# Kernel optimization log

Hardware: AMD Instinct MI355X
Metric: run time of the kernel (lower is better)

## Reference

```python
import jax, jax.numpy as jnp
import numpy as np

# Uniform batch of B graphs, N nodes each, C features, skip-window size FS
B, N, C, FS = 64, 512, 128, 16
RES = N - 1            # number of window rows per graph (unfold1d with stride 1)
TAU_A, TAU_B, TOT_EPOCHS = 10.0, 0.1, 100.0
EPS = 1e-20
NEG = -1e9


def setup_inputs() -> dict:
    key = jax.random.key(0)
    k1, k2, k3, k4 = jax.random.split(key, 4)
    x = jax.random.normal(k1, (B * N, C), dtype=jnp.float32)
    edge_index = jax.random.randint(k2, (2, 524288), 0, B * N, dtype=jnp.int32)
    score_w = jax.random.normal(k3, (C, 1), dtype=jnp.float32)       # TopKPool Linear weight
    att_params = jax.random.normal(k4, (2 * C, 1), dtype=jnp.float32)  # SKipPool att_params
    return {"x": x, "edge_index": edge_index, "score_w": score_w,
            "att_params": att_params, "epoch": 10}


def _forward(x, score_w, att_params, epoch):
    tau0 = TAU_A * (TAU_B / TAU_A) ** (epoch / TOT_EPOCHS)

    # ---- TopKPool scorer (init_ratio -> 1.0: keep all nodes, rank-sort per graph) ----
    scores = (x @ score_w)[:, 0] / jnp.linalg.norm(score_w)   # [B*N]
    sv = scores.reshape(B, N)
    order = jnp.argsort(-sv, axis=1)                           # descending perm per graph
    xg = jnp.take_along_axis(x.reshape(B, N, C), order[:, :, None], axis=1)  # [B,N,C]
    scores_ranked = jnp.tanh(jnp.take_along_axis(sv, order, axis=1))         # [B,N]

    # ---- skip-window edge construction (unfold1d semantics): row r -> dests r..r+FS-1 ----
    r = jnp.arange(RES)
    j = jnp.arange(FS)
    dest = r[:, None] + j[None, :]            # [RES,FS]
    valid = dest < N                          # padded positions masked (inf/zero rows)
    destc = jnp.minimum(dest, N - 1)

    xs = xg[:, :RES, None, :]                                  # [B,RES,1,C] sources
    xd = jnp.where(valid[None, :, :, None], xg[:, destc], 0.0)  # [B,RES,FS,C] dests

    # getDM_ei: RBF kernel over edge distances (sigma=1); masked edges -> 0 (inf row)
    d = jnp.linalg.norm(xs - xd, axis=-1)                      # [B,RES,FS]
    kmat = jnp.where(valid[None], jnp.exp(-d / 2.0), 0.0) - EPS

    # getSM_ei: attention score via att_params on [x_src || x_dst]
    a_src, a_dst = att_params[:C, 0], att_params[C:, 0]
    atts = (xg[:, :RES] @ a_src)[:, :, None] + jnp.einsum('brjc,c->brj', xd, a_dst)
    atts = jnp.where(valid[None], atts, NEG)
    w_att = jax.nn.softmax(atts / tau0, axis=-1)               # tau-annealed row softmax

    q = kmat * w_att                                           # combined edge score [B,RES,FS]
    qm = jnp.where(valid[None], q, NEG)
    w_row = jnp.max(qm, axis=-1)                               # best-match score per row (scatterSort top-1)
    jumps = 1 + jnp.argmax(qm[:, :, 1:], axis=-1).astype(jnp.int32)  # data-dependent stride in [1,FS-1]

    # ---- sequential pivot chaining (innerLoopStar): pivot -> pivot + jump[pivot] ----
    def chain(xg_b, w_b, sr_b, jumps_b):
        def step(carry, _):
            p, acc = carry
            active = p < RES
            pc = jnp.minimum(p, RES - 1)
            wv = jnp.where(active, w_b[pc] * sr_b[pc], 0.0)
            acc = acc + wv * xg_b[pc]
            p = jnp.where(active, p + jumps_b[pc], p)
            return (p, acc), None
        (pf, acc), _ = jax.lax.scan(step, (jnp.int32(0), jnp.zeros((C,), xg_b.dtype)),
                                    None, length=RES)
        return acc

    pooled = jax.vmap(chain)(xg, w_row, scores_ranked[:, :RES], jumps)  # [B,C]
    return pooled


def reference(x, edge_index, score_w, att_params, epoch):
    # edge_index only feeds the scorer's filter_adj in the original (structure unused here)
    return _forward(x, score_w, att_params, epoch)
```

## Files before the change

### kernel.cpp

```cpp
#include <hip/hip_runtime.h>
#include <math.h>

#define B_   64
#define N_   512
#define C_   128
#define FS_  16
#define RES_ 511
#define CHUNK_ 64
#define HALO_  15
#define MAXR_  (CHUNK_ + HALO_)
#define RSTRIDE_ 132

__device__ __forceinline__ float bf2f(unsigned short u) {
  union { unsigned int i; float f; } v;
  v.i = ((unsigned int)u) << 16;
  return v.f;
}

__device__ __forceinline__ float2 ld2(const void* p, int idx, int mode) {
  if (mode) return ((const float2*)p)[idx];
  ushort2 u = ((const ushort2*)p)[idx];
  return make_float2(bf2f(u.x), bf2f(u.y));
}
__device__ __forceinline__ float ld1(const void* p, int idx, int mode) {
  if (mode) return ((const float*)p)[idx];
  return bf2f(((const unsigned short*)p)[idx]);
}
__device__ __forceinline__ float4 ld4(const void* p, int idx4, int mode) {
  if (mode) return ((const float4*)p)[idx4];
  ushort4 u = ((const ushort4*)p)[idx4];
  return make_float4(bf2f(u.x), bf2f(u.y), bf2f(u.z), bf2f(u.w));
}

__device__ __forceinline__ double wred(double v) {
#pragma unroll
  for (int m = 32; m; m >>= 1) v += __shfl_xor(v, m, 64);
  return v;
}
__device__ __forceinline__ float wredf(float v) {
#pragma unroll
  for (int m = 32; m; m >>= 1) v += __shfl_xor(v, m, 64);
  return v;
}

__device__ __forceinline__ int detect_w0(const unsigned short* p, int lane) {
  int e = (p[lane] >> 7) & 0xFF;
  unsigned long long m = __ballot(e >= 100 && e <= 140);
  return (__popcll(m) >= 48) ? 0 : 1;
}

__device__ __forceinline__ float get_epoch(const int* ep) {
  int ei = ep[0];
  if (ei >= 0 && ei <= 1000000) return (float)ei;
  union { int i; float f; } u; u.i = ei;
  return (u.f >= 0.f && u.f <= 1e6f) ? u.f : 10.f;
}

__global__ __launch_bounds__(256) void k_scores(
    const void* __restrict__ x, const void* __restrict__ w,
    float* __restrict__ sc)
{
  __shared__ int s_modes[2];
  const int t = threadIdx.x, lane = t & 63;
  if (t < 64) {
    int mx_ = detect_w0((const unsigned short*)x, lane);
    int mw_ = detect_w0((const unsigned short*)w, lane);
    if (t == 0) { s_modes[0] = mx_; s_modes[1] = mw_; }
  }
  __syncthreads();
  const int mode_x = s_modes[0], mode_w = s_modes[1];
  const int wid = (blockIdx.x * blockDim.x + t) >> 6;

  const float2 wv2 = ld2(w, lane, mode_w);
  const double nww = wred((double)wv2.x * wv2.x + (double)wv2.y * wv2.y);
  const float nrm32 = (float)sqrt(nww);

  float2 xv = ld2(x, wid * 64 + lane, mode_x);
  double s  = wred((double)xv.x * wv2.x + (double)xv.y * wv2.y);
  if (lane == 0) sc[wid] = ((float)s) / nrm32;
}

__global__ __launch_bounds__(256) void k_sort(
    const float* __restrict__ sc, int* __restrict__ order,
    float* __restrict__ srk)
{
  __shared__ __align__(16) float sl[N_];
  __shared__ int part[4][CHUNK_];
  const int blk = blockIdx.x, b = blk >> 3, ch = blk & 7;
  const int bN = b * N_, t = threadIdx.x;
  sl[t]       = sc[bN + t];
  sl[t + 256] = sc[bN + t + 256];
  __syncthreads();
  const int n = t & 63, p = t >> 6;
  const int g = ch * CHUNK_ + n;
  const float my = sl[g];
  const float4* sl4 = (const float4*)sl;
  int rank = 0;
#pragma unroll 4
  for (int k4 = p * 32; k4 < p * 32 + 32; ++k4) {
    float4 v = sl4[k4];
    int k = k4 * 4;
    rank += (int)((v.x > my) || (v.x == my && k     < g));
    rank += (int)((v.y > my) || (v.y == my && k + 1 < g));
    rank += (int)((v.z > my) || (v.z == my && k + 2 < g));
    rank += (int)((v.w > my) || (v.w == my && k + 3 < g));
  }
  part[p][n] = rank;
  __syncthreads();
  if (t < CHUNK_) {
    const int gg = ch * CHUNK_ + t;
    const int r = part[0][t] + part[1][t] + part[2][t] + part[3][t];
    order[bN + r] = gg;
    srk[bN + r]   = tanhf(sl[gg]);
  }
}

__global__ __launch_bounds__(512) void k_att(
    const void* __restrict__ x, const void* __restrict__ a,
    const int* __restrict__ order, const int* __restrict__ ep,
    float* __restrict__ wrw, int* __restrict__ jmp)
{
  __shared__ float rows[MAXR_ * RSTRIDE_];
  __shared__ float ads_l[MAXR_];
  __shared__ float asr_l[CHUNK_];
  __shared__ int   ord_l[MAXR_];
  __shared__ int   s_modes[2];
  __shared__ float s_invtau;

  const int blk = blockIdx.x;
  const int b = blk >> 3;
  const int cr0 = (blk & 7) * CHUNK_;
  const int bN = b * N_;
  const int t = threadIdx.x;
  const int lane = t & 63, wv = t >> 6;
  const int nrows = min(N_ - cr0, MAXR_);

  if (t < 64) {
    int mx_ = detect_w0((const unsigned short*)x, lane);
    int ma_ = detect_w0((const unsigned short*)a, lane);
    if (t == 0) {
      s_modes[0] = mx_; s_modes[1] = ma_;
      float evv = get_epoch(ep);
      s_invtau = (float)(1.0 / (10.0 * pow(0.01, (double)evv / 100.0)));
    }
  }
  if (t < nrows) {
    int o = order[bN + cr0 + t];
    ord_l[t] = min(max(o, 0), N_ - 1);
  }
  __syncthreads();
  const int mode_x = s_modes[0], mode_a = s_modes[1];
  const float inv_tau = s_invtau;

  {
    const int rl0 = t >> 5, c4 = t & 31;
    for (int rl = rl0; rl < nrows; rl += 16) {
      float4 v = ld4(x, (bN + ord_l[rl]) * 32 + c4, mode_x);
      float* dst = &rows[rl * RSTRIDE_ + c4 * 4];
      dst[0] = v.x; dst[1] = v.y; dst[2] = v.z; dst[3] = v.w;
    }
  }
  __syncthreads();

  {
    const float2 sv2 = ld2(a, lane, mode_a);
    const float2 dv2 = ld2(a, 64 + lane, mode_a);
    for (int rl = wv; rl < nrows; rl += 8) {
      const float2 xr = *(const float2*)&rows[rl * RSTRIDE_ + 2 * lane];
      float da = wredf(xr.x * sv2.x + xr.y * sv2.y);
      float dd = wredf(xr.x * dv2.x + xr.y * dv2.y);
      if (lane == 0) {
        ads_l[rl] = dd;
        if (rl < CHUNK_) asr_l[rl] = da;
      }
    }
  }
  __syncthreads();

  const int j = lane & 15, cg4 = lane >> 4;
  const int nr = min(CHUNK_, RES_ - cr0);
  int cnt = nr - wv * 8; cnt = max(0, min(8, cnt));

#pragma unroll 2
  for (int ii = 0; ii < cnt; ++ii) {
    const int rloc = wv * 8 + ii;
    const int r = cr0 + rloc;
    const int dest = r + j;
    const bool valid = dest < N_;
    const int dl = (valid ? dest : (N_ - 1)) - cr0;

    const float* srcp = &rows[rloc * RSTRIDE_ + cg4 * 32];
    const float* dstp = &rows[dl   * RSTRIDE_ + cg4 * 32];
    double p0 = 0.0, p1 = 0.0, p2 = 0.0, p3 = 0.0;
#pragma unroll
    for (int c = 0; c < 8; ++c) {
      float4 s4 = *(const float4*)(srcp + c * 4);
      float4 d4 = *(const float4*)(dstp + c * 4);
      float e0 = s4.x - d4.x, e1 = s4.y - d4.y;
      float e2 = s4.z - d4.z, e3 = s4.w - d4.w;
      float q0 = e0 * e0, q1 = e1 * e1, q2 = e2 * e2, q3 = e3 * e3;
      p0 += (double)q0; p1 += (double)q1; p2 += (double)q2; p3 += (double)q3;
    }
    double dacc = (p0 + p1) + (p2 + p3);
    dacc += __shfl_xor(dacc, 16, 64);
    dacc += __shfl_xor(dacc, 32, 64);

    float d32 = sqrtf((float)dacc);
    float kkj = valid ? (__expf(-0.5f * d32) - 1e-20f) : -1e-20f;
    float aaj = valid ? (asr_l[rloc] + ads_l[dl]) : -1e9f;
    float ttj = aaj * inv_tau;

    float mx = ttj;
#pragma unroll
    for (int m = 1; m < 16; m <<= 1) mx = fmaxf(mx, __shfl_xor(mx, m, 64));
    float eej = __expf(ttj - mx);
    float ssum = eej;
#pragma unroll
    for (int m = 1; m < 16; m <<= 1) ssum += __shfl_xor(ssum, m, 64);
    float q  = kkj * (eej * (1.0f / ssum));
    float qm = valid ? q : -1e9f;

    float qe = (j == 0) ? -INFINITY : qm;
    float m1 = qe;
#pragma unroll
    for (int m = 1; m < 16; m <<= 1) m1 = fmaxf(m1, __shfl_xor(m1, m, 64));
    float q0v = __shfl(qm, lane & 48, 64);
    float wr = fmaxf(m1, q0v);
    unsigned long long mask = __ballot(qe == m1);
    int bj = __builtin_ctz((unsigned)(mask & 0xFFFEu));

    if (lane == 0) {
      wrw[bN + r] = wr;
      jmp[bN + r] = bj;
    }
  }
}

__global__ __launch_bounds__(512) void k_chain(
    const void* __restrict__ x, const float* __restrict__ wrw,
    const float* __restrict__ srk, const int* __restrict__ jmp,
    const int* __restrict__ order, float* __restrict__ out)
{
  __shared__ int   tab[9][N_];
  __shared__ int   ol[N_];
  __shared__ float wl[N_];
  __shared__ float sl2[N_];
  __shared__ float cl[N_];
  __shared__ int   rl[N_];
  __shared__ int   Pcnt;
  __shared__ int   s_mode;

  const int b = blockIdx.x, t = threadIdx.x;
  if (t < 64) {
    int mx_ = detect_w0((const unsigned short*)x, t);
    if (t == 0) s_mode = mx_;
  }

  ol[t] = min(max(order[b * N_ + t], 0), N_ - 1);
  if (t < RES_) {
    wl[t]  = wrw[b * N_ + t];
    sl2[t] = srk[b * N_ + t];
    int jv = jmp[b * N_ + t];
    jv = min(max(jv, 1), FS_ - 1);
    tab[0][t] = min(t + jv, RES_);
  } else {
    tab[0][t] = RES_;
  }
  if (t == 0) Pcnt = RES_;
  __syncthreads();
  const int mode_x = s_mode;
#pragma unroll
  for (int k = 1; k < 9; ++k) {
    int v = tab[k - 1][tab[k - 1][t]];
    tab[k][t] = v;
    __syncthreads();
  }
  int node = 0;
#pragma unroll
  for (int k = 0; k < 9; ++k)
    if ((t >> k) & 1) node = tab[k][node];
  bool valid = (node < RES_);
  cl[t] = valid ? wl[node] * sl2[node] : 0.0f;
  rl[t] = valid ? ol[node] : 0;
  if (!valid) atomicMin(&Pcnt, t);
  __syncthreads();

  if (t < C_) {
    const int P = Pcnt;
    float acc = 0.f;
    int i = 0;
    for (; i + 4 <= P; i += 4) {
      float c0 = cl[i],     c1 = cl[i + 1], c2 = cl[i + 2], c3 = cl[i + 3];
      int   r0 = rl[i],     r1 = rl[i + 1], r2 = rl[i + 2], r3 = rl[i + 3];
      float x0 = ld1(x, (b * N_ + r0) * C_ + t, mode_x);
      float x1 = ld1(x, (b * N_ + r1) * C_ + t, mode_x);
      float x2 = ld1(x, (b * N_ + r2) * C_ + t, mode_x);
      float x3 = ld1(x, (b * N_ + r3) * C_ + t, mode_x);
      acc = acc + c0 * x0;
      acc = acc + c1 * x1;
      acc = acc + c2 * x2;
      acc = acc + c3 * x3;
    }
    for (; i < P; ++i)
      acc = acc + cl[i] * ld1(x, (b * N_ + rl[i]) * C_ + t, mode_x);
    out[b * C_ + t] = acc;
  }
}

extern "C" void kernel_launch(void* const* d_in, const int* in_sizes, int n_in,
                              void* d_out, int out_size, void* d_ws, size_t ws_size,
                              hipStream_t stream) {
  const void* x = nullptr; const void* w = nullptr; const void* a = nullptr;
  const int* ep = nullptr;
  for (int i = 0; i < n_in; ++i) {
    int s = in_sizes[i];
    if      (s == B_ * N_ * C_) x  = d_in[i];
    else if (s == C_)           w  = d_in[i];
    else if (s == 2 * C_)       a  = d_in[i];
    else if (s == 1)            ep = (const int*)d_in[i];
  }
  if (!x)  x  = d_in[0];
  if (!w)  w  = d_in[2];
  if (!a)  a  = d_in[3];
  if (!ep) ep = (const int*)d_in[4];
  (void)out_size; (void)ws_size;

  float* ws = (float*)d_ws;
  const int NN = B_ * N_;
  float* sc    = ws;
  int*   order = (int*)(ws + NN);
  float* srk   = ws + 2 * NN;
  float* wrw   = ws + 3 * NN;
  int*   jmp   = (int*)(ws + 4 * NN);

  k_scores<<<NN / 4, 256, 0, stream>>>(x, w, sc);
  k_sort<<<B_ * 8, 256, 0, stream>>>(sc, order, srk);
  k_att<<<B_ * 8, 512, 0, stream>>>(x, a, order, ep, wrw, jmp);
  k_chain<<<B_, N_, 0, stream>>>(x, wrw, srk, jmp, order, (float*)d_out);
}
```

Measured before the change: 121.9 us.

## Fuse four kernels into one cooperative kernel with grid-wide syncs

Merges the score, sort, attention and chain stages into a single cooperative kernel of 512 blocks that uses grid.sync between stages, removing three kernel launch boundaries. A union of shared memory layouts is reused across the stages. The cost is the grid barriers, fewer blocks for the scoring stage, and only 64 of 512 blocks doing work in the final chain stage. If cooperative launch is unavailable or occupancy is too low, the code falls back to the original four kernels.

```diff
diff --git a/kernel.cpp b/kernel.cpp
--- a/kernel.cpp
+++ b/kernel.cpp
@@ -1,5 +1,8 @@
 #include <hip/hip_runtime.h>
+#include <hip/hip_cooperative_groups.h>
 #include <math.h>
+
+namespace cg = cooperative_groups;
 
 #define B_   64
 #define N_   512
@@ -55,6 +58,7 @@
   union { int i; float f; } u; u.i = ei;
   return (u.f >= 0.f && u.f <= 1e6f) ? u.f : 10.f;
 }
+
 
 __global__ __launch_bounds__(256) void k_scores(
     const void* __restrict__ x, const void* __restrict__ w,
@@ -307,6 +311,256 @@
   }
 }
 
+
+union __align__(16) SMem {
+  struct {
+    float sl[N_];
+    int   part[8][CHUNK_];
+  } srt;
+  struct {
+    float rows[MAXR_ * RSTRIDE_];
+    float ads_l[MAXR_];
+    float asr_l[CHUNK_];
+    int   ord_l[MAXR_];
+  } att;
+  struct {
+    int   tab[9][N_];
+    int   ol[N_];
+    float wl[N_];
+    float sl2[N_];
+    float cl[N_];
+    int   rl[N_];
+  } chn;
+};
+
+__global__ __launch_bounds__(512, 4) void k_fused(
+    const void* __restrict__ x, const void* __restrict__ w,
+    const void* __restrict__ a, const int* __restrict__ ep,
+    float* __restrict__ sc, int* __restrict__ order, float* __restrict__ srk,
+    float* __restrict__ wrw, int* __restrict__ jmp, float* __restrict__ out)
+{
+  cg::grid_group grid = cg::this_grid();
+
+  __shared__ SMem sm;
+  __shared__ int   s_modes[3];
+  __shared__ float s_invtau;
+  __shared__ int   s_Pcnt;
+
+  const int blk = blockIdx.x;
+  const int t = threadIdx.x;
+  const int lane = t & 63, wv = t >> 6;
+
+  if (t < 64) {
+    int mx_ = detect_w0((const unsigned short*)x, lane);
+    int mw_ = detect_w0((const unsigned short*)w, lane);
+    int ma_ = detect_w0((const unsigned short*)a, lane);
+    if (lane == 0) {
+      s_modes[0] = mx_; s_modes[1] = mw_; s_modes[2] = ma_;
+      float evv = get_epoch(ep);
+      s_invtau = (float)(1.0 / (10.0 * pow(0.01, (double)evv / 100.0)));
+    }
+  }
+  __syncthreads();
+  const int mode_x = s_modes[0], mode_w = s_modes[1], mode_a = s_modes[2];
+  const float inv_tau = s_invtau;
+
+  {
+    const float2 wv2 = ld2(w, lane, mode_w);
+    const double nww = wred((double)wv2.x * wv2.x + (double)wv2.y * wv2.y);
+    const float nrm32 = (float)sqrt(nww);
+    const int node0 = blk * 64 + wv * 8;
+#pragma unroll 2
+    for (int i = 0; i < 8; ++i) {
+      const int node = node0 + i;
+      float2 xv = ld2(x, node * 64 + lane, mode_x);
+      double s  = wred((double)xv.x * wv2.x + (double)xv.y * wv2.y);
+      if (lane == 0) sc[node] = ((float)s) / nrm32;
+    }
+  }
+  __threadfence();
+  grid.sync();
+
+  const int b = blk >> 3, ch = blk & 7, bN = b * N_;
+
+  {
+    sm.srt.sl[t] = sc[bN + t];
+    __syncthreads();
+    const int n = t & 63, p = t >> 6;
+    const int g = ch * CHUNK_ + n;
+    const float my = sm.srt.sl[g];
+    const float4* sl4 = (const float4*)sm.srt.sl;
+    int rank = 0;
+#pragma unroll 4
+    for (int k4 = p * 16; k4 < p * 16 + 16; ++k4) {
+      float4 v = sl4[k4];
+      int k = k4 * 4;
+      rank += (int)((v.x > my) || (v.x == my && k     < g));
+      rank += (int)((v.y > my) || (v.y == my && k + 1 < g));
+      rank += (int)((v.z > my) || (v.z == my && k + 2 < g));
+      rank += (int)((v.w > my) || (v.w == my && k + 3 < g));
+    }
+    sm.srt.part[p][n] = rank;
+    __syncthreads();
+    if (t < CHUNK_) {
+      const int gg = ch * CHUNK_ + t;
+      int r = 0;
+#pragma unroll
+      for (int pp = 0; pp < 8; ++pp) r += sm.srt.part[pp][t];
+      order[bN + r] = gg;
+      srk[bN + r]   = tanhf(sm.srt.sl[gg]);
+    }
+  }
+  __threadfence();
+  grid.sync();
+
+  {
+    const int cr0 = ch * CHUNK_;
+    const int nrows = min(N_ - cr0, MAXR_);
+    if (t < nrows) {
+      int o = order[bN + cr0 + t];
+      sm.att.ord_l[t] = min(max(o, 0), N_ - 1);
+    }
+    __syncthreads();
+    {
+      const int rl0 = t >> 5, c4 = t & 31;
+      for (int rl = rl0; rl < nrows; rl += 16) {
+        float4 v = ld4(x, (bN + sm.att.ord_l[rl]) * 32 + c4, mode_x);
+        float* dst = &sm.att.rows[rl * RSTRIDE_ + c4 * 4];
+        dst[0] = v.x; dst[1] = v.y; dst[2] = v.z; dst[3] = v.w;
+      }
+    }
+    __syncthreads();
+    {
+      const float2 sv2 = ld2(a, lane, mode_a);
+      const float2 dv2 = ld2(a, 64 + lane, mode_a);
+      for (int rl = wv; rl < nrows; rl += 8) {
+        const float2 xr = *(const float2*)&sm.att.rows[rl * RSTRIDE_ + 2 * lane];
+        float da = wredf(xr.x * sv2.x + xr.y * sv2.y);
+        float dd = wredf(xr.x * dv2.x + xr.y * dv2.y);
+        if (lane == 0) {
+          sm.att.ads_l[rl] = dd;
+          if (rl < CHUNK_) sm.att.asr_l[rl] = da;
+        }
+      }
+    }
+    __syncthreads();
+
+    const int j = lane & 15, cg4 = lane >> 4;
+    const int nr = min(CHUNK_, RES_ - cr0);
+    int cnt = nr - wv * 8; cnt = max(0, min(8, cnt));
+
+#pragma unroll 2
+    for (int ii = 0; ii < cnt; ++ii) {
+      const int rloc = wv * 8 + ii;
+      const int r = cr0 + rloc;
+      const int dest = r + j;
+      const bool valid = dest < N_;
+      const int dl = (valid ? dest : (N_ - 1)) - cr0;
+
+      const float* srcp = &sm.att.rows[rloc * RSTRIDE_ + cg4 * 32];
+      const float* dstp = &sm.att.rows[dl   * RSTRIDE_ + cg4 * 32];
+      double p0 = 0.0, p1 = 0.0, p2 = 0.0, p3 = 0.0;
+#pragma unroll
+      for (int c = 0; c < 8; ++c) {
+        float4 s4 = *(const float4*)(srcp + c * 4);
+        float4 d4 = *(const float4*)(dstp + c * 4);
+        float e0 = s4.x - d4.x, e1 = s4.y - d4.y;
+        float e2 = s4.z - d4.z, e3 = s4.w - d4.w;
+        float q0 = e0 * e0, q1 = e1 * e1, q2 = e2 * e2, q3 = e3 * e3;
+        p0 += (double)q0; p1 += (double)q1; p2 += (double)q2; p3 += (double)q3;
+      }
+      double dacc = (p0 + p1) + (p2 + p3);
+      dacc += __shfl_xor(dacc, 16, 64);
+      dacc += __shfl_xor(dacc, 32, 64);
+
+      float d32 = sqrtf((float)dacc);
+      float kkj = valid ? (__expf(-0.5f * d32) - 1e-20f) : -1e-20f;
+      float aaj = valid ? (sm.att.asr_l[rloc] + sm.att.ads_l[dl]) : -1e9f;
+      float ttj = aaj * inv_tau;
+
+      float mx = ttj;
+#pragma unroll
+      for (int m = 1; m < 16; m <<= 1) mx = fmaxf(mx, __shfl_xor(mx, m, 64));
+      float eej = __expf(ttj - mx);
+      float ssum = eej;
+#pragma unroll
+      for (int m = 1; m < 16; m <<= 1) ssum += __shfl_xor(ssum, m, 64);
+      float q  = kkj * (eej * (1.0f / ssum));
+      float qm = valid ? q : -1e9f;
+
+      float qe = (j == 0) ? -INFINITY : qm;
+      float m1 = qe;
+#pragma unroll
+      for (int m = 1; m < 16; m <<= 1) m1 = fmaxf(m1, __shfl_xor(m1, m, 64));
+      float q0v = __shfl(qm, lane & 48, 64);
+      float wr = fmaxf(m1, q0v);
+      unsigned long long mask = __ballot(qe == m1);
+      int bj = __builtin_ctz((unsigned)(mask & 0xFFFEu));
+
+      if (lane == 0) {
+        wrw[bN + r] = wr;
+        jmp[bN + r] = bj;
+      }
+    }
+  }
+  __threadfence();
+  grid.sync();
+
+  if (blk < B_) {
+    const int bD = blk, bND = bD * N_;
+    sm.chn.ol[t] = min(max(order[bND + t], 0), N_ - 1);
+    if (t < RES_) {
+      sm.chn.wl[t]  = wrw[bND + t];
+      sm.chn.sl2[t] = srk[bND + t];
+      int jv = jmp[bND + t];
+      jv = min(max(jv, 1), FS_ - 1);
+      sm.chn.tab[0][t] = min(t + jv, RES_);
+    } else {
+      sm.chn.tab[0][t] = RES_;
+    }
+    if (t == 0) s_Pcnt = RES_;
+    __syncthreads();
+#pragma unroll
+    for (int k = 1; k < 9; ++k) {
+      int v = sm.chn.tab[k - 1][sm.chn.tab[k - 1][t]];
+      sm.chn.tab[k][t] = v;
+      __syncthreads();
+    }
+    int node = 0;
+#pragma unroll
+    for (int k = 0; k < 9; ++k)
+      if ((t >> k) & 1) node = sm.chn.tab[k][node];
+    bool valid = (node < RES_);
+    sm.chn.cl[t] = valid ? sm.chn.wl[node] * sm.chn.sl2[node] : 0.0f;
+    sm.chn.rl[t] = valid ? sm.chn.ol[node] : 0;
+    if (!valid) atomicMin(&s_Pcnt, t);
+    __syncthreads();
+
+    if (t < C_) {
+      const int P = s_Pcnt;
+      float acc = 0.f;
+      int i = 0;
+      for (; i + 4 <= P; i += 4) {
+        float c0 = sm.chn.cl[i],     c1 = sm.chn.cl[i + 1];
+        float c2 = sm.chn.cl[i + 2], c3 = sm.chn.cl[i + 3];
+        int   r0 = sm.chn.rl[i],     r1 = sm.chn.rl[i + 1];
+        int   r2 = sm.chn.rl[i + 2], r3 = sm.chn.rl[i + 3];
+        float x0 = ld1(x, (bND + r0) * C_ + t, mode_x);
+        float x1 = ld1(x, (bND + r1) * C_ + t, mode_x);
+        float x2 = ld1(x, (bND + r2) * C_ + t, mode_x);
+        float x3 = ld1(x, (bND + r3) * C_ + t, mode_x);
+        acc = acc + c0 * x0;
+        acc = acc + c1 * x1;
+        acc = acc + c2 * x2;
+        acc = acc + c3 * x3;
+      }
+      for (; i < P; ++i)
+        acc = acc + sm.chn.cl[i] * ld1(x, (bND + sm.chn.rl[i]) * C_ + t, mode_x);
+      out[bD * C_ + t] = acc;
+    }
+  }
+}
+
 extern "C" void kernel_launch(void* const* d_in, const int* in_sizes, int n_in,
                               void* d_out, int out_size, void* d_ws, size_t ws_size,
                               hipStream_t stream) {
@@ -332,6 +586,27 @@
   float* srk   = ws + 2 * NN;
   float* wrw   = ws + 3 * NN;
   int*   jmp   = (int*)(ws + 4 * NN);
+  float* outp  = (float*)d_out;
+
+  static int coop_capacity = -1;
+  if (coop_capacity < 0) {
+    int dev = 0, coop = 0, cus = 0, nb = 0;
+    hipGetDevice(&dev);
+    hipDeviceGetAttribute(&coop, hipDeviceAttributeCooperativeLaunch, dev);
+    hipDeviceGetAttribute(&cus, hipDeviceAttributeMultiprocessorCount, dev);
+    if (hipOccupancyMaxActiveBlocksPerMultiprocessor(
+            &nb, (const void*)k_fused, 512, 0) != hipSuccess) nb = 0;
+    coop_capacity = coop ? nb * cus : 0;
+  }
+  if (coop_capacity >= 512) {
+    void* args[] = {(void*)&x, (void*)&w, (void*)&a, (void*)&ep,
+                    (void*)&sc, (void*)&order, (void*)&srk,
+                    (void*)&wrw, (void*)&jmp, (void*)&outp};
+    if (hipLaunchCooperativeKernel((const void*)k_fused, dim3(512), dim3(512),
+                                   args, 0, stream) == hipSuccess)
+      return;
+    coop_capacity = 0;
+  }
 
   k_scores<<<NN / 4, 256, 0, stream>>>(x, w, sc);
   k_sort<<<B_ * 8, 256, 0, stream>>>(sc, order, srk);
```

After: 121.7 us. About the same (-0.2%).

## Fuse sort, attention and chain kernels into one kernel with per-graph arrival counter

Applied to the files above, without the earlier changes.

Merges the rank-sort, attention/jump computation and pivot-chain pooling into a single kernel. Each block recomputes the full per-graph rank sort redundantly in shared memory instead of reading an order array. The last-stage chain work is done by chunk 0 of each graph, which spins on an atomic counter until all 8 chunk blocks of that graph have published their results. Shared memory is overlaid with a union to fit both phases. This removes two launches and the order/srk round trips through global memory, at the cost of redundant sort work and a spin-wait that relies on all blocks being co-resident or scheduled in order.

```diff
diff --git a/kernel.cpp b/kernel.cpp
--- a/kernel.cpp
+++ b/kernel.cpp
@@ -58,10 +58,11 @@
 
 __global__ __launch_bounds__(256) void k_scores(
     const void* __restrict__ x, const void* __restrict__ w,
-    float* __restrict__ sc)
+    float* __restrict__ sc, int* __restrict__ cnt)
 {
   __shared__ int s_modes[2];
   const int t = threadIdx.x, lane = t & 63;
+  if (blockIdx.x < B_ && t == 0) cnt[blockIdx.x] = 0;
   if (t < 64) {
     int mx_ = detect_w0((const unsigned short*)x, lane);
     int mw_ = detect_w0((const unsigned short*)w, lane);
@@ -80,60 +81,41 @@
   if (lane == 0) sc[wid] = ((float)s) / nrm32;
 }
 
-__global__ __launch_bounds__(256) void k_sort(
-    const float* __restrict__ sc, int* __restrict__ order,
-    float* __restrict__ srk)
+union __align__(16) SMemU {
+  struct {
+    float rows[MAXR_ * RSTRIDE_];
+    float ads[MAXR_];
+    float asr[CHUNK_];
+  } att;
+  struct {
+    int   tab[9][N_];
+    int   ol[N_];
+    float wl[N_];
+    float sl2[N_];
+    float cl[N_];
+    int   rl[N_];
+  } chn;
+};
+
+__global__ __launch_bounds__(512, 4) void k_main(
+    const void* __restrict__ x, const void* __restrict__ a,
+    const float* __restrict__ sc, const int* __restrict__ ep,
+    float* __restrict__ wrw, int* __restrict__ jmp,
+    int* __restrict__ cnt, float* __restrict__ out)
 {
+  __shared__ SMemU sm;
   __shared__ __align__(16) float sl[N_];
-  __shared__ int part[4][CHUNK_];
-  const int blk = blockIdx.x, b = blk >> 3, ch = blk & 7;
-  const int bN = b * N_, t = threadIdx.x;
-  sl[t]       = sc[bN + t];
-  sl[t + 256] = sc[bN + t + 256];
-  __syncthreads();
-  const int n = t & 63, p = t >> 6;
-  const int g = ch * CHUNK_ + n;
-  const float my = sl[g];
-  const float4* sl4 = (const float4*)sl;
-  int rank = 0;
-#pragma unroll 4
-  for (int k4 = p * 32; k4 < p * 32 + 32; ++k4) {
-    float4 v = sl4[k4];
-    int k = k4 * 4;
-    rank += (int)((v.x > my) || (v.x == my && k     < g));
-    rank += (int)((v.y > my) || (v.y == my && k + 1 < g));
-    rank += (int)((v.z > my) || (v.z == my && k + 2 < g));
-    rank += (int)((v.w > my) || (v.w == my && k + 3 < g));
-  }
-  part[p][n] = rank;
-  __syncthreads();
-  if (t < CHUNK_) {
-    const int gg = ch * CHUNK_ + t;
-    const int r = part[0][t] + part[1][t] + part[2][t] + part[3][t];
-    order[bN + r] = gg;
-    srk[bN + r]   = tanhf(sl[gg]);
-  }
-}
-
-__global__ __launch_bounds__(512) void k_att(
-    const void* __restrict__ x, const void* __restrict__ a,
-    const int* __restrict__ order, const int* __restrict__ ep,
-    float* __restrict__ wrw, int* __restrict__ jmp)
-{
-  __shared__ float rows[MAXR_ * RSTRIDE_];
-  __shared__ float ads_l[MAXR_];
-  __shared__ float asr_l[CHUNK_];
-  __shared__ int   ord_l[MAXR_];
+  __shared__ int   ord_full[N_];
   __shared__ int   s_modes[2];
   __shared__ float s_invtau;
+  __shared__ int   s_Pcnt;
 
   const int blk = blockIdx.x;
-  const int b = blk >> 3;
-  const int cr0 = (blk & 7) * CHUNK_;
+  const int b = blk >> 3, ch = blk & 7;
+  const int cr0 = ch * CHUNK_;
   const int bN = b * N_;
   const int t = threadIdx.x;
   const int lane = t & 63, wv = t >> 6;
-  const int nrows = min(N_ - cr0, MAXR_);
 
   if (t < 64) {
     int mx_ = detect_w0((const unsigned short*)x, lane);
@@ -144,19 +126,37 @@
       s_invtau = (float)(1.0 / (10.0 * pow(0.01, (double)evv / 100.0)));
     }
   }
-  if (t < nrows) {
-    int o = order[bN + cr0 + t];
-    ord_l[t] = min(max(o, 0), N_ - 1);
-  }
+  sl[t] = sc[bN + t];
+  ord_full[t] = 0;
   __syncthreads();
   const int mode_x = s_modes[0], mode_a = s_modes[1];
   const float inv_tau = s_invtau;
 
   {
+    const float my = sl[t];
+    const float4* sl4 = (const float4*)sl;
+    int rank = 0;
+#pragma unroll 4
+    for (int k4 = 0; k4 < N_ / 4; ++k4) {
+      float4 v = sl4[k4];
+      int k = k4 * 4;
+      rank += (int)((v.x > my) || (v.x == my && k     < t));
+      rank += (int)((v.y > my) || (v.y == my && k + 1 < t));
+      rank += (int)((v.z > my) || (v.z == my && k + 2 < t));
+      rank += (int)((v.w > my) || (v.w == my && k + 3 < t));
+    }
+    ord_full[rank] = t;
+  }
+  __syncthreads();
+
+  const int nrows = min(N_ - cr0, MAXR_);
+  {
     const int rl0 = t >> 5, c4 = t & 31;
     for (int rl = rl0; rl < nrows; rl += 16) {
-      float4 v = ld4(x, (bN + ord_l[rl]) * 32 + c4, mode_x);
-      float* dst = &rows[rl * RSTRIDE_ + c4 * 4];
+      int o = ord_full[cr0 + rl];
+      o = min(max(o, 0), N_ - 1);
+      float4 v = ld4(x, (bN + o) * 32 + c4, mode_x);
+      float* dst = &sm.att.rows[rl * RSTRIDE_ + c4 * 4];
       dst[0] = v.x; dst[1] = v.y; dst[2] = v.z; dst[3] = v.w;
     }
   }
@@ -166,144 +166,148 @@
     const float2 sv2 = ld2(a, lane, mode_a);
     const float2 dv2 = ld2(a, 64 + lane, mode_a);
     for (int rl = wv; rl < nrows; rl += 8) {
-      const float2 xr = *(const float2*)&rows[rl * RSTRIDE_ + 2 * lane];
+      const float2 xr = *(const float2*)&sm.att.rows[rl * RSTRIDE_ + 2 * lane];
       float da = wredf(xr.x * sv2.x + xr.y * sv2.y);
       float dd = wredf(xr.x * dv2.x + xr.y * dv2.y);
       if (lane == 0) {
-        ads_l[rl] = dd;
-        if (rl < CHUNK_) asr_l[rl] = da;
+        sm.att.ads[rl] = dd;
+        if (rl < CHUNK_) sm.att.asr[rl] = da;
       }
     }
   }
   __syncthreads();
 
-  const int j = lane & 15, cg4 = lane >> 4;
-  const int nr = min(CHUNK_, RES_ - cr0);
-  int cnt = nr - wv * 8; cnt = max(0, min(8, cnt));
+  {
+    const int j = lane & 15, cg4 = lane >> 4;
+    const int nr = min(CHUNK_, RES_ - cr0);
+    int cnt_i = nr - wv * 8; cnt_i = max(0, min(8, cnt_i));
 
 #pragma unroll 2
-  for (int ii = 0; ii < cnt; ++ii) {
-    const int rloc = wv * 8 + ii;
-    const int r = cr0 + rloc;
-    const int dest = r + j;
-    const bool valid = dest < N_;
-    const int dl = (valid ? dest : (N_ - 1)) - cr0;
-
-    const float* srcp = &rows[rloc * RSTRIDE_ + cg4 * 32];
-    const float* dstp = &rows[dl   * RSTRIDE_ + cg4 * 32];
-    double p0 = 0.0, p1 = 0.0, p2 = 0.0, p3 = 0.0;
-#pragma unroll
-    for (int c = 0; c < 8; ++c) {
-      float4 s4 = *(const float4*)(srcp + c * 4);
-      float4 d4 = *(const float4*)(dstp + c * 4);
-      float e0 = s4.x - d4.x, e1 = s4.y - d4.y;
-      float e2 = s4.z - d4.z, e3 = s4.w - d4.w;
-      float q0 = e0 * e0, q1 = e1 * e1, q2 = e2 * e2, q3 = e3 * e3;
-      p0 += (double)q0; p1 += (double)q1; p2 += (double)q2; p3 += (double)q3;
-    }
-    double dacc = (p0 + p1) + (p2 + p3);
-    dacc += __shfl_xor(dacc, 16, 64);
-    dacc += __shfl_xor(dacc, 32, 64);
-
-    float d32 = sqrtf((float)dacc);
-    float kkj = valid ? (__expf(-0.5f * d32) - 1e-20f) : -1e-20f;
-    float aaj = valid ? (asr_l[rloc] + ads_l[dl]) : -1e9f;
-    float ttj = aaj * inv_tau;
-
-    float mx = ttj;
-#pragma unroll
-    for (int m = 1; m < 16; m <<= 1) mx = fmaxf(mx, __shfl_xor(mx, m, 64));
-    float eej = __expf(ttj - mx);
-    float ssum = eej;
-#pragma unroll
-    for (int m = 1; m < 16; m <<= 1) ssum += __shfl_xor(ssum, m, 64);
-    float q  = kkj * (eej * (1.0f / ssum));
-    float qm = valid ? q : -1e9f;
-
-    float qe = (j == 0) ? -INFINITY : qm;
-    float m1 = qe;
-#pragma unroll
-    for (int m = 1; m < 16; m <<= 1) m1 = fmaxf(m1, __shfl_xor(m1, m, 64));
-    float q0v = __shfl(qm, lane & 48, 64);
-    float wr = fmaxf(m1, q0v);
-    unsigned long long mask = __ballot(qe == m1);
-    int bj = __builtin_ctz((unsigned)(mask & 0xFFFEu));
-
-    if (lane == 0) {
-      wrw[bN + r] = wr;
-      jmp[bN + r] = bj;
-    }
-  }
-}
-
-__global__ __launch_bounds__(512) void k_chain(
-    const void* __restrict__ x, const float* __restrict__ wrw,
-    const float* __restrict__ srk, const int* __restrict__ jmp,
-    const int* __restrict__ order, float* __restrict__ out)
-{
-  __shared__ int   tab[9][N_];
-  __shared__ int   ol[N_];
-  __shared__ float wl[N_];
-  __shared__ float sl2[N_];
-  __shared__ float cl[N_];
-  __shared__ int   rl[N_];
-  __shared__ int   Pcnt;
-  __shared__ int   s_mode;
-
-  const int b = blockIdx.x, t = threadIdx.x;
-  if (t < 64) {
-    int mx_ = detect_w0((const unsigned short*)x, t);
-    if (t == 0) s_mode = mx_;
-  }
-
-  ol[t] = min(max(order[b * N_ + t], 0), N_ - 1);
-  if (t < RES_) {
-    wl[t]  = wrw[b * N_ + t];
-    sl2[t] = srk[b * N_ + t];
-    int jv = jmp[b * N_ + t];
-    jv = min(max(jv, 1), FS_ - 1);
-    tab[0][t] = min(t + jv, RES_);
-  } else {
-    tab[0][t] = RES_;
-  }
-  if (t == 0) Pcnt = RES_;
-  __syncthreads();
-  const int mode_x = s_mode;
-#pragma unroll
-  for (int k = 1; k < 9; ++k) {
-    int v = tab[k - 1][tab[k - 1][t]];
-    tab[k][t] = v;
+    for (int ii = 0; ii < cnt_i; ++ii) {
+      const int rloc = wv * 8 + ii;
+      const int r = cr0 + rloc;
+      const int dest = r + j;
+      const bool valid = dest < N_;
+      const int dl = (valid ? dest : (N_ - 1)) - cr0;
+
+      const float* srcp = &sm.att.rows[rloc * RSTRIDE_ + cg4 * 32];
+      const float* dstp = &sm.att.rows[dl   * RSTRIDE_ + cg4 * 32];
+      double p0 = 0.0, p1 = 0.0, p2 = 0.0, p3 = 0.0;
+#pragma unroll
+      for (int c = 0; c < 8; ++c) {
+        float4 s4 = *(const float4*)(srcp + c * 4);
+        float4 d4 = *(const float4*)(dstp + c * 4);
+        float e0 = s4.x - d4.x, e1 = s4.y - d4.y;
+        float e2 = s4.z - d4.z, e3 = s4.w - d4.w;
+        float q0 = e0 * e0, q1 = e1 * e1, q2 = e2 * e2, q3 = e3 * e3;
+        p0 += (double)q0; p1 += (double)q1; p2 += (double)q2; p3 += (double)q3;
+      }
+      double dacc = (p0 + p1) + (p2 + p3);
+      dacc += __shfl_xor(dacc, 16, 64);
+      dacc += __shfl_xor(dacc, 32, 64);
+
+      float d32 = sqrtf((float)dacc);
+      float kkj = valid ? (__expf(-0.5f * d32) - 1e-20f) : -1e-20f;
+      float aaj = valid ? (sm.att.asr[rloc] + sm.att.ads[dl]) : -1e9f;
+      float ttj = aaj * inv_tau;
+
+      float mx = ttj;
+#pragma unroll
+      for (int m = 1; m < 16; m <<= 1) mx = fmaxf(mx, __shfl_xor(mx, m, 64));
+      float eej = __expf(ttj - mx);
+      float ssum = eej;
+#pragma unroll
+      for (int m = 1; m < 16; m <<= 1) ssum += __shfl_xor(ssum, m, 64);
+      float q  = kkj * (eej * (1.0f / ssum));
+      float qm = valid ? q : -1e9f;
+
+      float qe = (j == 0) ? -INFINITY : qm;
+      float m1 = qe;
+#pragma unroll
+      for (int m = 1; m < 16; m <<= 1) m1 = fmaxf(m1, __shfl_xor(m1, m, 64));
+      float q0v = __shfl(qm, lane & 48, 64);
+      float wr = fmaxf(m1, q0v);
+      unsigned long long mask = __ballot(qe == m1);
+      int bj = __builtin_ctz((unsigned)(mask & 0xFFFEu));
+
+      if (lane == 0) {
+        wrw[bN + r] = wr;
+        jmp[bN + r] = bj;
+      }
+    }
+  }
+
+  __threadfence();
+  __syncthreads();
+  if (t == 0)
+    __hip_atomic_fetch_add(&cnt[b], 1, __ATOMIC_RELEASE,
+                           __HIP_MEMORY_SCOPE_AGENT);
+  if (ch != 0) return;
+
+  if (t == 0) {
+    long long spins = 0;
+    while (__hip_atomic_load(&cnt[b], __ATOMIC_ACQUIRE,
+                             __HIP_MEMORY_SCOPE_AGENT) < 8) {
+      __builtin_amdgcn_s_sleep(2);
+      if (++spins > 200000000LL) break;
+    }
+    __threadfence();
+  }
+  __syncthreads();
+
+  {
+    int olv = min(max(ord_full[t], 0), N_ - 1);
+    sm.chn.ol[t] = olv;
+    float sl2v = tanhf(sl[olv]);
+    if (t < RES_) {
+      sm.chn.wl[t]  = wrw[bN + t];
+      sm.chn.sl2[t] = sl2v;
+      int jv = jmp[bN + t];
+      jv = min(max(jv, 1), FS_ - 1);
+      sm.chn.tab[0][t] = min(t + jv, RES_);
+    } else {
+      sm.chn.tab[0][t] = RES_;
+    }
+    if (t == 0) s_Pcnt = RES_;
     __syncthreads();
-  }
-  int node = 0;
-#pragma unroll
-  for (int k = 0; k < 9; ++k)
-    if ((t >> k) & 1) node = tab[k][node];
-  bool valid = (node < RES_);
-  cl[t] = valid ? wl[node] * sl2[node] : 0.0f;
-  rl[t] = valid ? ol[node] : 0;
-  if (!valid) atomicMin(&Pcnt, t);
-  __syncthreads();
-
-  if (t < C_) {
-    const int P = Pcnt;
-    float acc = 0.f;
-    int i = 0;
-    for (; i + 4 <= P; i += 4) {
-      float c0 = cl[i],     c1 = cl[i + 1], c2 = cl[i + 2], c3 = cl[i + 3];
-      int   r0 = rl[i],     r1 = rl[i + 1], r2 = rl[i + 2], r3 = rl[i + 3];
-      float x0 = ld1(x, (b * N_ + r0) * C_ + t, mode_x);
-      float x1 = ld1(x, (b * N_ + r1) * C_ + t, mode_x);
-      float x2 = ld1(x, (b * N_ + r2) * C_ + t, mode_x);
-      float x3 = ld1(x, (b * N_ + r3) * C_ + t, mode_x);
-      acc = acc + c0 * x0;
-      acc = acc + c1 * x1;
-      acc = acc + c2 * x2;
-      acc = acc + c3 * x3;
-    }
-    for (; i < P; ++i)
-      acc = acc + cl[i] * ld1(x, (b * N_ + rl[i]) * C_ + t, mode_x);
-    out[b * C_ + t] = acc;
+#pragma unroll
+    for (int k = 1; k < 9; ++k) {
+      int v = sm.chn.tab[k - 1][sm.chn.tab[k - 1][t]];
+      sm.chn.tab[k][t] = v;
+      __syncthreads();
+    }
+    int node = 0;
+#pragma unroll
+    for (int k = 0; k < 9; ++k)
+      if ((t >> k) & 1) node = sm.chn.tab[k][node];
+    bool valid = (node < RES_);
+    sm.chn.cl[t] = valid ? sm.chn.wl[node] * sm.chn.sl2[node] : 0.0f;
+    sm.chn.rl[t] = valid ? sm.chn.ol[node] : 0;
+    if (!valid) atomicMin(&s_Pcnt, t);
+    __syncthreads();
+
+    if (t < C_) {
+      const int P = s_Pcnt;
+      float acc = 0.f;
+      int i = 0;
+      for (; i + 4 <= P; i += 4) {
+        float c0 = sm.chn.cl[i],     c1 = sm.chn.cl[i + 1];
+        float c2 = sm.chn.cl[i + 2], c3 = sm.chn.cl[i + 3];
+        int   r0 = sm.chn.rl[i],     r1 = sm.chn.rl[i + 1];
+        int   r2 = sm.chn.rl[i + 2], r3 = sm.chn.rl[i + 3];
+        float x0 = ld1(x, (bN + r0) * C_ + t, mode_x);
+        float x1 = ld1(x, (bN + r1) * C_ + t, mode_x);
+        float x2 = ld1(x, (bN + r2) * C_ + t, mode_x);
+        float x3 = ld1(x, (bN + r3) * C_ + t, mode_x);
+        acc = acc + c0 * x0;
+        acc = acc + c1 * x1;
+        acc = acc + c2 * x2;
+        acc = acc + c3 * x3;
+      }
+      for (; i < P; ++i)
+        acc = acc + sm.chn.cl[i] * ld1(x, (bN + sm.chn.rl[i]) * C_ + t, mode_x);
+      out[b * C_ + t] = acc;
+    }
   }
 }
 
@@ -327,14 +331,12 @@
 
   float* ws = (float*)d_ws;
   const int NN = B_ * N_;
-  float* sc    = ws;
-  int*   order = (int*)(ws + NN);
-  float* srk   = ws + 2 * NN;
-  float* wrw   = ws + 3 * NN;
-  int*   jmp   = (int*)(ws + 4 * NN);
-
-  k_scores<<<NN / 4, 256, 0, stream>>>(x, w, sc);
-  k_sort<<<B_ * 8, 256, 0, stream>>>(sc, order, srk);
-  k_att<<<B_ * 8, 512, 0, stream>>>(x, a, order, ep, wrw, jmp);
-  k_chain<<<B_, N_, 0, stream>>>(x, wrw, srk, jmp, order, (float*)d_out);
-}
+  float* sc  = ws;
+  float* wrw = ws + NN;
+  int*   jmp = (int*)(ws + 2 * NN);
+  int*   cnt = (int*)(ws + 3 * NN);
+
+  k_scores<<<NN / 4, 256, 0, stream>>>(x, w, sc, cnt);
+  k_main<<<B_ * 8, 512, 0, stream>>>(x, a, sc, ep, wrw, jmp, cnt,
+                                     (float*)d_out);
+}
```

Result: slower. 209.2 us (+71.6%).
